# Kernel optimization log

Hardware: AMD Instinct MI355X
Metric: run time of the kernel (lower is better)

## Reference

```python
import jax, jax.numpy as jnp
import numpy as np

B, N, C = 4, 8192, 512
H = 4
D = C // H  # 128
HID = 4 * C  # mlp hidden, mlp_ratio=4.0
SCALE = D ** -0.5
EPS = 1e-5


def layernorm(x, w, b):
    mu = jnp.mean(x, axis=-1, keepdims=True)
    var = jnp.var(x, axis=-1, keepdims=True)
    return (x - mu) * jax.lax.rsqrt(var + EPS) * w + b


def setup_inputs() -> dict:
    key = jax.random.key(0)
    ks = jax.random.split(key, 8)
    s = lambda fan_in: 1.0 / np.sqrt(fan_in)
    return {
        "x": jax.random.normal(ks[0], (B, N, C), jnp.float32),
        "norm1_w": jnp.ones((C,), jnp.float32),
        "norm1_b": jnp.zeros((C,), jnp.float32),
        "qkv_w": jax.random.normal(ks[1], (C, 3 * C), jnp.float32) * s(C),
        "qkv_b": jnp.zeros((3 * C,), jnp.float32),
        "lnk_w": jnp.ones((D,), jnp.float32),
        "lnk_b": jnp.zeros((D,), jnp.float32),
        "lnv_w": jnp.ones((D,), jnp.float32),
        "lnv_b": jnp.zeros((D,), jnp.float32),
        "proj_w": jax.random.normal(ks[2], (C, C), jnp.float32) * s(C),
        "proj_b": jnp.zeros((C,), jnp.float32),
        "norm2_w": jnp.ones((C,), jnp.float32),
        "norm2_b": jnp.zeros((C,), jnp.float32),
        "mlp_w1": jax.random.normal(ks[3], (C, HID), jnp.float32) * s(C),
        "mlp_b1": jnp.zeros((HID,), jnp.float32),
        "mlp_w2": jax.random.normal(ks[4], (HID, C), jnp.float32) * s(HID),
        "mlp_b2": jnp.zeros((C,), jnp.float32),
    }


def reference(x, norm1_w, norm1_b, qkv_w, qkv_b, lnk_w, lnk_b, lnv_w, lnv_b,
              proj_w, proj_b, norm2_w, norm2_b, mlp_w1, mlp_b1, mlp_w2, mlp_b2):
    shortcut = x
    xn = layernorm(x, norm1_w, norm1_b)
    qkv = xn @ qkv_w + qkv_b                       # [B,N,3C]
    qkv = qkv.reshape(B, N, 3, H, D).transpose(2, 0, 3, 1, 4)  # [3,B,H,N,D]
    q, k, v = qkv[0], qkv[1], qkv[2]
    k = layernorm(k, lnk_w, lnk_b)
    v = layernorm(v, lnv_w, lnv_b)
    context = jnp.einsum('bhnd,bhne->bhde', k, v)   # [B,H,D,D] small context
    attn = jnp.einsum('bhnd,bhde->bhne', q, context) * SCALE  # [B,H,N,D]
    attn = attn.transpose(0, 2, 1, 3).reshape(B, N, C)
    x1 = shortcut + (attn @ proj_w + proj_b)
    h = layernorm(x1, norm2_w, norm2_b)
    mlp = jax.nn.gelu(h @ mlp_w1 + mlp_b1, approximate=False) @ mlp_w2 + mlp_b2
    return x1 + mlp
```

## Files before the change

kernel.cpp:

```cpp
#include <hip/hip_runtime.h>
#include <stdint.h>


#define B_    4
#define N_    8192
#define C_    512
#define H_    4
#define D_    128
#define HID_  2048
#define M_    (B_*N_)
#define EPS_  1e-5f
#define SCALE_ 0.08838834764831845f

typedef unsigned short u16;
typedef __attribute__((ext_vector_type(8))) __bf16 bfrag_t;
typedef __attribute__((ext_vector_type(4))) float  f4_t;

__device__ __forceinline__ float bf2f(u16 a) {
    unsigned int u = ((unsigned int)a) << 16; float f;
    __builtin_memcpy(&f, &u, 4); return f;
}
__device__ __forceinline__ u16 f2bf(float f) {
    unsigned int u; __builtin_memcpy(&u, &f, 4);
    u += 0x7FFFu + ((u >> 16) & 1u);
    return (u16)(u >> 16);
}
__device__ __forceinline__ u16 f2bf_fast(float f) {
    unsigned int u; __builtin_memcpy(&u, &f, 4);
    return (u16)((u + 0x8000u) >> 16);
}

__device__ __forceinline__ float fast_gelu(float x) {
    const float kA = 2.3022084f;
    const float kB = 0.1029435f;
    float x2 = x * x;
    float e1 = __builtin_amdgcn_exp2f(x * (kB * x2 + kA));
    return x - x * __builtin_amdgcn_rcpf(e1 + 1.0f);
}

__device__ __forceinline__ void gld16(u16* lds, const u16* g) {
    void* gp = const_cast<u16*>(g);
    __builtin_amdgcn_global_load_lds((__attribute__((address_space(1))) void*)gp,
                                     (__attribute__((address_space(3))) void*)lds,
                                     16, 0, 0);
}

__global__ void wtrans(const float* __restrict__ in, u16* __restrict__ out,
                       int K, int Ncols) {
    long idx = (long)blockIdx.x * 256 + threadIdx.x;
    long total = (long)K * Ncols;
    if (idx >= total) return;
    int k = (int)(idx % K), n = (int)(idx / K);
    out[idx] = f2bf(in[(long)k * Ncols + n]);
}

__global__ __launch_bounds__(256)
void ln_rows(const float* __restrict__ in, const float* __restrict__ w,
             const float* __restrict__ b, u16* __restrict__ out) {
    long row = blockIdx.x;
    int t = threadIdx.x;
    const float* p = in + row * 512;
    float v0 = p[t], v1 = p[t + 256];
    float s = v0 + v1, q = v0 * v0 + v1 * v1;
    #pragma unroll
    for (int o = 32; o >= 1; o >>= 1) { s += __shfl_xor(s, o, 64); q += __shfl_xor(q, o, 64); }
    __shared__ float sh[8];
    int wv = t >> 6, l = t & 63;
    if (l == 0) { sh[wv] = s; sh[4 + wv] = q; }
    __syncthreads();
    s = sh[0] + sh[1] + sh[2] + sh[3];
    q = sh[4] + sh[5] + sh[6] + sh[7];
    float mu = s * (1.f / 512.f);
    float var = q * (1.f / 512.f) - mu * mu;
    float rs = rsqrtf(var + EPS_);
    out[row * 512 + t]       = f2bf((v0 - mu) * rs * w[t] + b[t]);
    out[row * 512 + t + 256] = f2bf((v1 - mu) * rs * w[t + 256] + b[t + 256]);
}

__global__ __launch_bounds__(256)
void lnkv(const u16* __restrict__ qkv,
          const float* __restrict__ kw, const float* __restrict__ kb,
          const float* __restrict__ vw, const float* __restrict__ vb,
          u16* __restrict__ kT, u16* __restrict__ vT) {
    int bh = blockIdx.x;
    int b = bh >> 2, h = bh & 3;
    int n0 = blockIdx.y * 64;
    int wv = threadIdx.x >> 6, l = threadIdx.x & 63;
    __shared__ u16 lk[128 * 68], lv[128 * 68];

    for (int r = wv; r < 64; r += 4) {
        long base = ((long)b * N_ + n0 + r) * 1536 + h * 128;
        {
            float x0 = bf2f(qkv[base + 512 + l]), x1 = bf2f(qkv[base + 512 + 64 + l]);
            float s = x0 + x1, q = x0 * x0 + x1 * x1;
            #pragma unroll
            for (int o = 32; o >= 1; o >>= 1) { s += __shfl_xor(s, o, 64); q += __shfl_xor(q, o, 64); }
            float mu = s * (1.f / 128.f), var = q * (1.f / 128.f) - mu * mu;
            float rs = rsqrtf(var + EPS_);
            lk[l * 68 + r]        = f2bf((x0 - mu) * rs * kw[l] + kb[l]);
            lk[(l + 64) * 68 + r] = f2bf((x1 - mu) * rs * kw[l + 64] + kb[l + 64]);
        }
        {
            float x0 = bf2f(qkv[base + 1024 + l]), x1 = bf2f(qkv[base + 1024 + 64 + l]);
            float s = x0 + x1, q = x0 * x0 + x1 * x1;
            #pragma unroll
            for (int o = 32; o >= 1; o >>= 1) { s += __shfl_xor(s, o, 64); q += __shfl_xor(q, o, 64); }
            float mu = s * (1.f / 128.f), var = q * (1.f / 128.f) - mu * mu;
            float rs = rsqrtf(var + EPS_);
            lv[l * 68 + r]        = f2bf((x0 - mu) * rs * vw[l] + vb[l]);
            lv[(l + 64) * 68 + r] = f2bf((x1 - mu) * rs * vw[l + 64] + vb[l + 64]);
        }
    }
    __syncthreads();
    long obase = (long)bh * D_ * N_;
    #pragma unroll 4
    for (int i = 0; i < 32; i++) {
        int idx = i * 256 + threadIdx.x;
        int d = idx >> 6, nn = idx & 63;
        kT[obase + (long)d * N_ + n0 + nn] = lk[d * 68 + nn];
        vT[obase + (long)d * N_ + n0 + nn] = lv[d * 68 + nn];
    }
}

__global__ void ctxfin(const float* __restrict__ ctx, u16* __restrict__ ctxT) {
    int idx = blockIdx.x * 256 + threadIdx.x;
    if (idx >= 16 * 16384) return;
    int z = idx >> 14, r = idx & 16383;
    int e = r >> 7, d = r & 127;
    ctxT[idx] = f2bf(ctx[(z << 14) + (d << 7) + e] * SCALE_);
}

template<int MODE, int KTOT, int ZDIV>
__global__ __launch_bounds__(256)
void gemm_bt(const u16* __restrict__ A, int lda, int64_t aZ1, int64_t aZ2,
             const u16* __restrict__ Bt, int ldb, int64_t bZ1, int64_t bZ2,
             void* __restrict__ outv, int ldo, int64_t oZ1, int64_t oZ2,
             const float* __restrict__ bias, const float* __restrict__ resid, int ldr) {
    __shared__ __align__(16) u16 sA[128 * 32];
    __shared__ __align__(16) u16 sB[128 * 32];
    const int z = blockIdx.z;
    const int z1 = z / ZDIV, z2 = z % ZDIV;
    A  += z1 * aZ1 + z2 * aZ2;
    Bt += z1 * bZ1 + z2 * bZ2;
    const int64_t ooff = z1 * oZ1 + z2 * oZ2;
    const int m0 = blockIdx.x * 128, n0 = blockIdx.y * 128;
    const int tid = threadIdx.x, wave = tid >> 6, lane = tid & 63;
    const int wr = wave >> 1, wc = wave & 1;

    f4_t acc[4][4];
    #pragma unroll
    for (int i = 0; i < 4; i++)
        #pragma unroll
        for (int j = 0; j < 4; j++) acc[i][j] = (f4_t){0.f, 0.f, 0.f, 0.f};

    const int c0 = wave * 64 + lane, c1 = 256 + wave * 64 + lane;
    const int r0 = c0 >> 2, e0 = (c0 & 3) * 8;
    const int r1 = c1 >> 2, e1 = (c1 & 3) * 8;
    const u16* a0 = A + (int64_t)(m0 + r0) * lda + e0;
    const u16* a1 = A + (int64_t)(m0 + r1) * lda + e1;
    const u16* b0 = Bt + (int64_t)(n0 + r0) * ldb + e0;
    const u16* b1 = Bt + (int64_t)(n0 + r1) * ldb + e1;
    u16* lA0 = &sA[wave * 512];        u16* lA1 = &sA[2048 + wave * 512];
    u16* lB0 = &sB[wave * 512];        u16* lB1 = &sB[2048 + wave * 512];

    const int qd = lane >> 4, md = lane & 15;
    int aoff[4], boff[4];
    #pragma unroll
    for (int i = 0; i < 4; i++) {
        aoff[i] = (wr * 64 + i * 16 + md) * 32 + qd * 8;
        boff[i] = (wc * 64 + i * 16 + md) * 32 + qd * 8;
    }

    #pragma unroll 4
    for (int kt = 0; kt < KTOT; kt += 32) {
        __syncthreads();
        gld16(lA0, a0 + kt);  gld16(lA1, a1 + kt);
        gld16(lB0, b0 + kt);  gld16(lB1, b1 + kt);
        __syncthreads();
        bfrag_t af[4], bf[4];
        #pragma unroll
        for (int i = 0; i < 4; i++) af[i] = *(const bfrag_t*)&sA[aoff[i]];
        #pragma unroll
        for (int i = 0; i < 4; i++) bf[i] = *(const bfrag_t*)&sB[boff[i]];
        #pragma unroll
        for (int mi = 0; mi < 4; mi++)
            #pragma unroll
            for (int ni = 0; ni < 4; ni++)
                acc[mi][ni] = __builtin_amdgcn_mfma_f32_16x16x32_bf16(
                    af[mi], bf[ni], acc[mi][ni], 0, 0, 0);
    }

    #pragma unroll
    for (int mi = 0; mi < 4; mi++) {
        #pragma unroll
        for (int r = 0; r < 4; r++) {
            int m = m0 + wr * 64 + mi * 16 + qd * 4 + r;
            int64_t rowo = ooff + (int64_t)m * ldo;
            #pragma unroll
            for (int ni = 0; ni < 4; ni++) {
                int n = n0 + wc * 64 + ni * 16 + md;
                float v = acc[mi][ni][r];
                if (MODE == 0)
                    ((u16*)outv)[rowo + n] = f2bf_fast(v);
                else
                    atomicAdd(&((float*)outv)[rowo + n], v);
            }
        }
    }
}

#define LD_(p)      (*(const bfrag_t*)(p))
#define FENCE_      asm volatile("" ::: "memory")
#define BAR_        do { FENCE_; __builtin_amdgcn_s_barrier(); FENCE_; } while (0)
#define WVM4_       asm volatile("s_waitcnt vmcnt(4)" ::: "memory")
#define WVM0_       asm volatile("s_waitcnt vmcnt(0)" ::: "memory")
#define MFMA_(va, vb, c) c = __builtin_amdgcn_mfma_f32_16x16x32_bf16(va, vb, c, 0, 0, 0)
#define MM16_(I0) do { __builtin_amdgcn_s_setprio(1); \
  MFMA_(a0,b0,acc[(I0)+0][0]); MFMA_(a0,b1,acc[(I0)+0][1]); MFMA_(a0,b2,acc[(I0)+0][2]); MFMA_(a0,b3,acc[(I0)+0][3]); \
  MFMA_(a1,b0,acc[(I0)+1][0]); MFMA_(a1,b1,acc[(I0)+1][1]); MFMA_(a1,b2,acc[(I0)+1][2]); MFMA_(a1,b3,acc[(I0)+1][3]); \
  MFMA_(a2,b0,acc[(I0)+2][0]); MFMA_(a2,b1,acc[(I0)+2][1]); MFMA_(a2,b2,acc[(I0)+2][2]); MFMA_(a2,b3,acc[(I0)+2][3]); \
  MFMA_(a3,b0,acc[(I0)+3][0]); MFMA_(a3,b1,acc[(I0)+3][1]); MFMA_(a3,b2,acc[(I0)+3][2]); MFMA_(a3,b3,acc[(I0)+3][3]); \
  __builtin_amdgcn_s_setprio(0); } while (0)
#define STGA_(nb, kk, tt) do { \
  u16* d_ = lds + (nb) * 32768 + (kk) * 8192 + wid * 512; \
  const u16* s_ = aS + (int64_t)(tt) * 64 + (kk) * 32; \
  gld16(d_, s_); gld16(d_ + 4096, s_ + a128); } while (0)
#define STGB_(nb, kk, tt) do { \
  u16* d_ = lds + (nb) * 32768 + 16384 + (kk) * 8192 + wid * 512; \
  const u16* s_ = bS + (int64_t)(tt) * 64 + (kk) * 32; \
  gld16(d_, s_); gld16(d_ + 4096, s_ + b128); } while (0)

template<int MODE, int KTOT>
__global__ __launch_bounds__(512, 2)
void gemm256(const u16* __restrict__ A, int lda,
             const u16* __restrict__ Bt, int ldb,
             void* __restrict__ outv, int ldo,
             const float* __restrict__ bias, const float* __restrict__ resid, int ldr) {
    __shared__ __align__(16) u16 lds[65536];
    const int gx = gridDim.x, gy = gridDim.y;
    const int lid = blockIdx.x + blockIdx.y * gx;
    int bx, by;
    if ((gx & 7) == 0) {
        const int j = lid >> 3;
        bx = (gx >> 3) * (lid & 7) + j / gy;
        by = j % gy;
    } else { bx = blockIdx.x; by = blockIdx.y; }
    const int m0 = bx * 256, n0 = by * 256;
    const int tid = threadIdx.x, wid = tid >> 6, lane = tid & 63;
    const int wr = wid >> 2, wc = wid & 3;
    const int md = lane & 15, qd = lane >> 4;

    f4_t acc[8][4];
    #pragma unroll
    for (int i = 0; i < 8; ++i)
        #pragma unroll
        for (int j = 0; j < 4; ++j) acc[i][j] = (f4_t){0.f, 0.f, 0.f, 0.f};

    const int srow = tid >> 2;
    const int scol = ((tid & 3) ^ ((tid >> 3) & 3)) * 8;
    const u16* aS = A  + (int64_t)(m0 + srow) * lda + scol;
    const u16* bS = Bt + (int64_t)(n0 + srow) * ldb + scol;
    const int64_t a128 = (int64_t)lda * 128, b128 = (int64_t)ldb * 128;

    const int xq = (qd ^ ((md >> 1) & 3)) * 16;
    const int aRow = (wr * 128 + md) * 64;
    const int bRow = (wc * 64 + md) * 64;
    const char* ldsc = (const char*)lds;

    constexpr int NT = KTOT / 64;

    {
        STGA_(0, 0, 0); STGB_(0, 0, 0); STGA_(0, 1, 0); STGB_(0, 1, 0);
        WVM4_; BAR_;
    }

    #pragma unroll 2
    for (int t = 0; t < NT; ++t) {
        const int cur = t & 1, nb = cur ^ 1;
        const char* cA = ldsc + cur * 65536 + aRow;
        const char* cB = ldsc + cur * 65536 + 32768 + bRow;
        const bool st = (t + 1 < NT);
        bfrag_t a0, a1, a2, a3, b0, b1, b2, b3;

        a0 = LD_(cA + xq);        a1 = LD_(cA + 1024 + xq);
        a2 = LD_(cA + 2048 + xq); a3 = LD_(cA + 3072 + xq);
        b0 = LD_(cB + xq);        b1 = LD_(cB + 1024 + xq);
        b2 = LD_(cB + 2048 + xq); b3 = LD_(cB + 3072 + xq);
        if (st) STGA_(nb, 0, t + 1);
        BAR_;
        MM16_(0);

        a0 = LD_(cA + 4096 + xq); a1 = LD_(cA + 5120 + xq);
        a2 = LD_(cA + 6144 + xq); a3 = LD_(cA + 7168 + xq);
        if (st) STGB_(nb, 0, t + 1);
        BAR_;
        MM16_(4);

        if (st) { WVM4_; } else { WVM0_; }
        BAR_;

        a0 = LD_(cA + 16384 + xq);        a1 = LD_(cA + 17408 + xq);
        a2 = LD_(cA + 18432 + xq);        a3 = LD_(cA + 19456 + xq);
        b0 = LD_(cB + 16384 + xq);        b1 = LD_(cB + 17408 + xq);
        b2 = LD_(cB + 18432 + xq);        b3 = LD_(cB + 19456 + xq);
        if (st) STGA_(nb, 1, t + 1);
        BAR_;
        MM16_(0);

        a0 = LD_(cA + 20480 + xq); a1 = LD_(cA + 21504 + xq);
        a2 = LD_(cA + 22528 + xq); a3 = LD_(cA + 23552 + xq);
        if (st) STGB_(nb, 1, t + 1);
        BAR_;
        MM16_(4);

        if (st) { WVM4_; } else { WVM0_; }
        BAR_;
    }

    #pragma unroll
    for (int i = 0; i < 8; ++i) {
        #pragma unroll
        for (int rr = 0; rr < 4; ++rr) {
            const int m = m0 + wr * 128 + i * 16 + qd * 4 + rr;
            const int64_t rowo = (int64_t)m * ldo;
            #pragma unroll
            for (int j = 0; j < 4; ++j) {
                const int n = n0 + wc * 64 + j * 16 + md;
                float v = acc[i][j][rr];
                if (MODE == 1 || MODE == 2 || MODE == 3) v += bias[n];
                if (MODE == 2) v = fast_gelu(v);
                if (MODE == 3) v += resid[(int64_t)m * ldr + n];
                if (MODE == 3)
                    ((float*)outv)[rowo + n] = v;
                else
                    ((u16*)outv)[rowo + n] = f2bf_fast(v);
            }
        }
    }
}

#undef LD_
#undef FENCE_
#undef BAR_
#undef WVM4_
#undef WVM0_
#undef MFMA_
#undef MM16_
#undef STGA_
#undef STGB_

extern "C" void kernel_launch(void* const* d_in, const int* in_sizes, int n_in,
                              void* d_out, int out_size, void* d_ws, size_t ws_size,
                              hipStream_t stream) {
    const float* x      = (const float*)d_in[0];
    const float* n1w    = (const float*)d_in[1];
    const float* n1b    = (const float*)d_in[2];
    const float* qkv_w  = (const float*)d_in[3];
    const float* qkv_b  = (const float*)d_in[4];
    const float* lnk_w  = (const float*)d_in[5];
    const float* lnk_b  = (const float*)d_in[6];
    const float* lnv_w  = (const float*)d_in[7];
    const float* lnv_b  = (const float*)d_in[8];
    const float* proj_w = (const float*)d_in[9];
    const float* proj_b = (const float*)d_in[10];
    const float* n2w    = (const float*)d_in[11];
    const float* n2b    = (const float*)d_in[12];
    const float* w1     = (const float*)d_in[13];
    const float* b1     = (const float*)d_in[14];
    const float* w2     = (const float*)d_in[15];
    const float* b2     = (const float*)d_in[16];
    float* out = (float*)d_out;

    char* ws = (char*)d_ws;
    u16*  qkvWT = (u16*)(ws + 0);
    u16*  projT = (u16*)(ws + 1572864);
    u16*  w1T   = (u16*)(ws + 2097152);
    u16*  w2T   = (u16*)(ws + 4194304);
    float* ctx  = (float*)(ws + 6291456);
    u16*  ctxT  = (u16*)(ws + 7340032);
    u16*  bufA  = (u16*)(ws + 7864320);
    u16*  qkv   = (u16*)(ws + 41418752);
    u16*  hid   = (u16*)(ws + 41418752);
    u16*  kT    = (u16*)(ws + 142082048);
    u16*  vT    = (u16*)(ws + 175636480);

    dim3 blk(256);
    dim3 blk5(512);

    wtrans<<<dim3(512 * 1536 / 256), blk, 0, stream>>>(qkv_w, qkvWT, 512, 1536);
    wtrans<<<dim3(512 * 512 / 256),  blk, 0, stream>>>(proj_w, projT, 512, 512);
    wtrans<<<dim3(512 * 2048 / 256), blk, 0, stream>>>(w1, w1T, 512, 2048);
    wtrans<<<dim3(2048 * 512 / 256), blk, 0, stream>>>(w2, w2T, 2048, 512);

    ln_rows<<<dim3(M_), blk, 0, stream>>>(x, n1w, n1b, bufA);

    gemm256<1, 512><<<dim3(M_ / 256, 1536 / 256), blk5, 0, stream>>>(
        bufA, 512, qkvWT, 512, (void*)qkv, 1536, qkv_b, nullptr, 0);

    lnkv<<<dim3(B_ * H_, N_ / 64), blk, 0, stream>>>(qkv, lnk_w, lnk_b, lnv_w, lnv_b, kT, vT);

    hipMemsetAsync(ctx, 0, 16 * 128 * 128 * 4, stream);
    gemm_bt<4, 512, 16><<<dim3(1, 1, B_ * H_ * 16), blk, 0, stream>>>(
        kT, N_, (int64_t)D_ * N_, 512,  vT, N_, (int64_t)D_ * N_, 512,
        (void*)ctx, 128, 16384, 0,  nullptr, nullptr, 0);
    ctxfin<<<dim3(16 * 16384 / 256), blk, 0, stream>>>(ctx, ctxT);

    gemm_bt<0, 128, 4><<<dim3(N_ / 128, 1, B_ * H_), blk, 0, stream>>>(
        qkv, 1536, (int64_t)N_ * 1536, 128,  ctxT, 128, 4 * 16384, 16384,
        (void*)bufA, 512, (int64_t)N_ * 512, 128,  nullptr, nullptr, 0);

    gemm256<3, 512><<<dim3(M_ / 256, 512 / 256), blk5, 0, stream>>>(
        bufA, 512, projT, 512, (void*)out, 512, proj_b, x, 512);

    ln_rows<<<dim3(M_), blk, 0, stream>>>(out, n2w, n2b, bufA);

    gemm256<2, 512><<<dim3(M_ / 256, HID_ / 256), blk5, 0, stream>>>(
        bufA, 512, w1T, 512, (void*)hid, HID_, b1, nullptr, 0);

    gemm256<3, 2048><<<dim3(M_ / 256, 512 / 256), blk5, 0, stream>>>(
        hid, HID_, w2T, HID_, (void*)out, 512, b2, out, 512);
}
```

Baseline: 562.5 us.

## Fold context matrix into projection weights and replace atomic split-K with partial sums

Result: slower. 574.7 us (+2.2%).

```diff
diff --git a/kernel.cpp b/kernel.cpp
--- a/kernel.cpp
+++ b/kernel.cpp
@@ -122,12 +122,15 @@
     }
 }
 
-__global__ void ctxfin(const float* __restrict__ ctx, u16* __restrict__ ctxT) {
+__global__ void ctxfin(const float* __restrict__ ctxP, u16* __restrict__ ctxN) {
     int idx = blockIdx.x * 256 + threadIdx.x;
     if (idx >= 16 * 16384) return;
-    int z = idx >> 14, r = idx & 16383;
-    int e = r >> 7, d = r & 127;
-    ctxT[idx] = f2bf(ctx[(z << 14) + (d << 7) + e] * SCALE_);
+    int bh = idx >> 14, r = idx & 16383;
+    const float* p = ctxP + (long)bh * 262144 + r;
+    float s = 0.f;
+    #pragma unroll
+    for (int q = 0; q < 16; q++) s += p[q * 16384];
+    ctxN[idx] = f2bf(s * SCALE_);
 }
 
 template<int MODE, int KTOT, int ZDIV>
@@ -203,7 +206,7 @@
                 if (MODE == 0)
                     ((u16*)outv)[rowo + n] = f2bf_fast(v);
                 else
-                    atomicAdd(&((float*)outv)[rowo + n], v);
+                    ((float*)outv)[rowo + n] = v;
             }
         }
     }
@@ -232,11 +235,15 @@
 
 template<int MODE, int KTOT>
 __global__ __launch_bounds__(512, 2)
-void gemm256(const u16* __restrict__ A, int lda,
-             const u16* __restrict__ Bt, int ldb,
-             void* __restrict__ outv, int ldo,
+void gemm256(const u16* __restrict__ A, int lda, int64_t aZ,
+             const u16* __restrict__ Bt, int ldb, int64_t bZ,
+             void* __restrict__ outv, int ldo, int64_t oZ,
              const float* __restrict__ bias, const float* __restrict__ resid, int ldr) {
     __shared__ __align__(16) u16 lds[65536];
+    const int z = blockIdx.z;
+    A += (int64_t)z * aZ;
+    Bt += (int64_t)z * bZ;
+    const int64_t ooff = (int64_t)z * oZ;
     const int gx = gridDim.x, gy = gridDim.y;
     const int lid = blockIdx.x + blockIdx.y * gx;
     int bx, by;
@@ -322,14 +329,14 @@
         #pragma unroll
         for (int rr = 0; rr < 4; ++rr) {
             const int m = m0 + wr * 128 + i * 16 + qd * 4 + rr;
-            const int64_t rowo = (int64_t)m * ldo;
+            const int64_t rowo = ooff + (int64_t)m * ldo;
             #pragma unroll
             for (int j = 0; j < 4; ++j) {
                 const int n = n0 + wc * 64 + j * 16 + md;
                 float v = acc[i][j][rr];
                 if (MODE == 1 || MODE == 2 || MODE == 3) v += bias[n];
                 if (MODE == 2) v = fast_gelu(v);
-                if (MODE == 3) v += resid[(int64_t)m * ldr + n];
+                if (MODE == 3) v += resid[ooff + (int64_t)m * ldr + n];
                 if (MODE == 3)
                     ((float*)outv)[rowo + n] = v;
                 else
@@ -376,13 +383,14 @@
     u16*  projT = (u16*)(ws + 1572864);
     u16*  w1T   = (u16*)(ws + 2097152);
     u16*  w2T   = (u16*)(ws + 4194304);
-    float* ctx  = (float*)(ws + 6291456);
-    u16*  ctxT  = (u16*)(ws + 7340032);
+    u16*  ctxN  = (u16*)(ws + 7340032);
     u16*  bufA  = (u16*)(ws + 7864320);
     u16*  qkv   = (u16*)(ws + 41418752);
     u16*  hid   = (u16*)(ws + 41418752);
     u16*  kT    = (u16*)(ws + 142082048);
     u16*  vT    = (u16*)(ws + 175636480);
+    float* ctxP = (float*)(ws + 7864320);
+    u16*  wqT   = (u16*)(ws + 7864320 + 16777216);
 
     dim3 blk(256);
     dim3 blk5(512);
@@ -394,29 +402,29 @@
 
     ln_rows<<<dim3(M_), blk, 0, stream>>>(x, n1w, n1b, bufA);
 
-    gemm256<1, 512><<<dim3(M_ / 256, 1536 / 256), blk5, 0, stream>>>(
-        bufA, 512, qkvWT, 512, (void*)qkv, 1536, qkv_b, nullptr, 0);
+    gemm256<1, 512><<<dim3(M_ / 256, 1536 / 256, 1), blk5, 0, stream>>>(
+        bufA, 512, 0, qkvWT, 512, 0, (void*)qkv, 1536, 0, qkv_b, nullptr, 0);
 
     lnkv<<<dim3(B_ * H_, N_ / 64), blk, 0, stream>>>(qkv, lnk_w, lnk_b, lnv_w, lnv_b, kT, vT);
 
-    hipMemsetAsync(ctx, 0, 16 * 128 * 128 * 4, stream);
-    gemm_bt<4, 512, 16><<<dim3(1, 1, B_ * H_ * 16), blk, 0, stream>>>(
+    gemm_bt<5, 512, 16><<<dim3(1, 1, B_ * H_ * 16), blk, 0, stream>>>(
         kT, N_, (int64_t)D_ * N_, 512,  vT, N_, (int64_t)D_ * N_, 512,
-        (void*)ctx, 128, 16384, 0,  nullptr, nullptr, 0);
-    ctxfin<<<dim3(16 * 16384 / 256), blk, 0, stream>>>(ctx, ctxT);
-
-    gemm_bt<0, 128, 4><<<dim3(N_ / 128, 1, B_ * H_), blk, 0, stream>>>(
-        qkv, 1536, (int64_t)N_ * 1536, 128,  ctxT, 128, 4 * 16384, 16384,
-        (void*)bufA, 512, (int64_t)N_ * 512, 128,  nullptr, nullptr, 0);
-
-    gemm256<3, 512><<<dim3(M_ / 256, 512 / 256), blk5, 0, stream>>>(
-        bufA, 512, projT, 512, (void*)out, 512, proj_b, x, 512);
+        (void*)ctxP, 128, 262144, 16384,  nullptr, nullptr, 0);
+    ctxfin<<<dim3(16 * 16384 / 256), blk, 0, stream>>>(ctxP, ctxN);
+
+    gemm_bt<0, 128, 4><<<dim3(4, 1, 16), blk, 0, stream>>>(
+        projT, 512, 0, 128,  ctxN, 128, 65536, 16384,
+        (void*)wqT, 512, 262144, 128,  nullptr, nullptr, 0);
+
+    gemm256<3, 512><<<dim3(N_ / 256, 512 / 256, B_), blk5, 0, stream>>>(
+        qkv, 1536, (int64_t)N_ * 1536,  wqT, 512, 262144,
+        (void*)out, 512, (int64_t)N_ * 512,  proj_b, x, 512);
 
     ln_rows<<<dim3(M_), blk, 0, stream>>>(out, n2w, n2b, bufA);
 
-    gemm256<2, 512><<<dim3(M_ / 256, HID_ / 256), blk5, 0, stream>>>(
-        bufA, 512, w1T, 512, (void*)hid, HID_, b1, nullptr, 0);
-
-    gemm256<3, 2048><<<dim3(M_ / 256, 512 / 256), blk5, 0, stream>>>(
-        hid, HID_, w2T, HID_, (void*)out, 512, b2, out, 512);
-}
+    gemm256<2, 512><<<dim3(M_ / 256, HID_ / 256, 1), blk5, 0, stream>>>(
+        bufA, 512, 0, w1T, 512, 0, (void*)hid, HID_, 0, b1, nullptr, 0);
+
+    gemm256<3, 2048><<<dim3(M_ / 256, 512 / 256, 1), blk5, 0, stream>>>(
+        hid, HID_, 0, w2T, HID_, 0, (void*)out, 512, 0, b2, out, 512);
+}
```
